# Kernel tuning notes

Hardware: AMD Instinct MI355X
Metric: run time of the kernel (lower is better)

The kernel has to match this reference:

```python
import jax, jax.numpy as jnp
import numpy as np

LN_EPS = 1e-5


def setup_inputs() -> dict:
    key = jax.random.key(0)
    k1, k2 = jax.random.split(key, 2)
    B, C, D, H, W = 2, 96, 32, 128, 128
    out_dim = 2 * C
    x = jax.random.normal(k1, (B, C, D, H, W), dtype=jnp.float32)
    # nn.Linear(8*C, out_dim, bias=False): weight shape (out_dim, 8*C)
    w = jax.random.normal(k2, (out_dim, 8 * C), dtype=jnp.float32) * 0.02
    gamma = jnp.ones((8 * C,), dtype=jnp.float32)
    beta = jnp.zeros((8 * C,), dtype=jnp.float32)
    return {"x": x, "w": w, "gamma": gamma, "beta": beta}


def reference(x, w, gamma, beta):
    B, C, D, H, W = x.shape
    D2, H2, W2 = D // 2, H // 2, W // 2
    # Strided 2x2x2 gather: reshape then move (dd,hh,ww) offsets next to C.
    # torch.cat order [x0..x7] = (dd,hh,ww) lexicographic, dd most significant,
    # with C channels per block -> layout (..., dd, hh, ww, C) flattened.
    xr = x.reshape(B, C, D2, 2, H2, 2, W2, 2)
    xr = xr.transpose(0, 2, 4, 6, 3, 5, 7, 1)  # (B, D2, H2, W2, dd, hh, ww, C)
    xf = xr.reshape(B, D2, H2, W2, 8 * C)
    # LayerNorm over last dim
    mu = jnp.mean(xf, axis=-1, keepdims=True)
    xc = xf - mu
    var = jnp.mean(xc * xc, axis=-1, keepdims=True)
    xn = xc * jax.lax.rsqrt(var + LN_EPS) * gamma + beta
    # Linear (no bias): y = xn @ w.T
    y = jnp.einsum('bdhwc,oc->bdhwo', xn, w)
    # back to channels-first (B, out_dim, D2, H2, W2)
    return y.transpose(0, 4, 1, 2, 3)
```

## Files before the change

### kernel.cpp

```cpp
#include <hip/hip_runtime.h>
#include <hip/hip_bf16.h>

typedef __attribute__((ext_vector_type(8))) short short8;
typedef __attribute__((ext_vector_type(4))) float f32x4;

#define LN_EPS 1e-5f

__device__ __forceinline__ unsigned short f2bf(float f) {
  union { float f; unsigned u; } v; v.f = f;
  unsigned r = v.u + 0x7FFFu + ((v.u >> 16) & 1u);
  return (unsigned short)(r >> 16);
}

__device__ __forceinline__ int a_addr(int row, int colb) {
  return row * 1536 + (colb ^ ((row & 7) << 4));
}


__global__ __launch_bounds__(256) void pm_prep(
    const float* __restrict__ w, const float* __restrict__ g,
    const float* __restrict__ be, unsigned short* __restrict__ wg,
    float* __restrict__ sb) {
  const int o = blockIdx.x;
  const int t = threadIdx.x;
  __shared__ float red[256][2];
  float sa = 0.f, ba = 0.f;
#pragma unroll
  for (int u = 0; u < 3; ++u) {
    int kp = t + 256 * u;
    int dh = kp / 192;
    int rem = kp - dh * 192;
    int c = rem >> 1, ww = rem & 1;
    int k = dh * 192 + ww * 96 + c;
    float wv = w[o * 768 + k];
    float v = wv * g[k];
    sa += v;
    ba += wv * be[k];
    int NT = o >> 4, ks = kp >> 5, qq = (kp >> 3) & 3, jj = kp & 7;
    wg[(((NT * 24 + ks) * 64) + qq * 16 + (o & 15)) * 8 + jj] = f2bf(v);
  }
  red[t][0] = sa; red[t][1] = ba;
  __syncthreads();
  if (t == 0) {
    float S = 0.f, B = 0.f;
    for (int i = 0; i < 256; ++i) { S += red[i][0]; B += red[i][1]; }
    sb[o] = S; sb[192 + o] = B;
  }
}

__global__ __launch_bounds__(256, 4) void pm_main(
    const float* __restrict__ x, const unsigned short* __restrict__ wg,
    const float* __restrict__ sb, float* __restrict__ out) {
  const int bid = blockIdx.x;
  const int wh = bid & 1;
  const int h2 = (bid >> 1) & 63;
  const int d2 = (bid >> 7) & 15;
  const int b = bid >> 11;
  const int t = threadIdx.x;
  const int lane = t & 63, wv = t >> 6;
  const int q = lane & 15, sc = lane >> 4;

  __shared__ __align__(16) unsigned char A_lds[32 * 1536];
  __shared__ float stats[32][2];
  __shared__ float part[4][32][2];

  const float* xb = x + (size_t)b * (96 * 32 * 128 * 128);
  const int dd = wv >> 1, hh = wv & 1;
  const int drow = 2 * d2 + dd, hrow = 2 * h2 + hh;

  float sum0 = 0.f, sq0 = 0.f, sum1 = 0.f, sq1 = 0.f;
#pragma unroll 4
  for (int cg = 0; cg < 12; ++cg) {
    int r0 = cg * 8 + 2 * sc;
    const float* p = xb + ((size_t)(r0 * 32 + drow) * 128 + hrow) * 128 + wh * 64 + 4 * q;
    float4 f0 = *(const float4*)p;
    float4 f1 = *(const float4*)(p + 32 * 128 * 128);
    sum0 += (f0.x + f0.y) + (f1.x + f1.y);
    sq0  += f0.x * f0.x + f0.y * f0.y + f1.x * f1.x + f1.y * f1.y;
    sum1 += (f0.z + f0.w) + (f1.z + f1.w);
    sq1  += f0.z * f0.z + f0.w * f0.w + f1.z * f1.z + f1.w * f1.w;
    int colb = 2 * (wv * 192 + cg * 16 + 4 * sc);
    ushort4 v0 = make_ushort4(f2bf(f0.x), f2bf(f0.y), f2bf(f1.x), f2bf(f1.y));
    ushort4 v1 = make_ushort4(f2bf(f0.z), f2bf(f0.w), f2bf(f1.z), f2bf(f1.w));
    *(ushort4*)&A_lds[a_addr(2 * q, colb)] = v0;
    *(ushort4*)&A_lds[a_addr(2 * q + 1, colb)] = v1;
  }
  sum0 += __shfl_xor(sum0, 16); sum0 += __shfl_xor(sum0, 32);
  sq0  += __shfl_xor(sq0, 16);  sq0  += __shfl_xor(sq0, 32);
  sum1 += __shfl_xor(sum1, 16); sum1 += __shfl_xor(sum1, 32);
  sq1  += __shfl_xor(sq1, 16);  sq1  += __shfl_xor(sq1, 32);
  if (sc == 0) {
    part[wv][2 * q][0] = sum0;     part[wv][2 * q][1] = sq0;
    part[wv][2 * q + 1][0] = sum1; part[wv][2 * q + 1][1] = sq1;
  }
  __syncthreads();
  if (t < 32) {
    float S = 0.f, Q = 0.f;
#pragma unroll
    for (int w4 = 0; w4 < 4; ++w4) { S += part[w4][t][0]; Q += part[w4][t][1]; }
    float mu = S * (1.f / 768.f);
    float var = Q * (1.f / 768.f) - mu * mu;
    float rs = rsqrtf(var + LN_EPS);
    stats[t][0] = rs;
    stats[t][1] = mu * rs;
  }
  __syncthreads();

  const int al = lane & 15, ah = lane >> 4;
  f32x4 acc[2][3];
#pragma unroll
  for (int mt = 0; mt < 2; ++mt)
#pragma unroll
    for (int nt = 0; nt < 3; ++nt) acc[mt][nt] = {0.f, 0.f, 0.f, 0.f};

  const short8* wgs = (const short8*)wg;
#pragma unroll 2
  for (int ks = 0; ks < 24; ++ks) {
    short8 afr[2];
#pragma unroll
    for (int mt = 0; mt < 2; ++mt)
      afr[mt] = *(const short8*)&A_lds[a_addr(mt * 16 + al, ks * 64 + ah * 16)];
#pragma unroll
    for (int nt = 0; nt < 3; ++nt) {
      short8 bfr = wgs[((wv * 3 + nt) * 24 + ks) * 64 + lane];
#pragma unroll
      for (int mt = 0; mt < 2; ++mt)
        acc[mt][nt] = __builtin_amdgcn_mfma_f32_16x16x32_bf16(afr[mt], bfr, acc[mt][nt], 0, 0, 0);
    }
  }

#pragma unroll
  for (int nt = 0; nt < 3; ++nt) {
    int o = wv * 48 + nt * 16 + al;
    float Sv = sb[o], Bv = sb[192 + o];
    float* ob = out + (((size_t)(b * 192 + o) * 16 + d2) * 64 + h2) * 64 + wh * 32;
#pragma unroll
    for (int mt = 0; mt < 2; ++mt) {
      int m0 = mt * 16 + ah * 4;
      float4 y;
      y.x = stats[m0 + 0][0] * acc[mt][nt][0] - stats[m0 + 0][1] * Sv + Bv;
      y.y = stats[m0 + 1][0] * acc[mt][nt][1] - stats[m0 + 1][1] * Sv + Bv;
      y.z = stats[m0 + 2][0] * acc[mt][nt][2] - stats[m0 + 2][1] * Sv + Bv;
      y.w = stats[m0 + 3][0] * acc[mt][nt][3] - stats[m0 + 3][1] * Sv + Bv;
      *(float4*)(ob + m0) = y;
    }
  }
}

extern "C" void kernel_launch(void* const* d_in, const int* in_sizes, int n_in,
                              void* d_out, int out_size, void* d_ws, size_t ws_size,
                              hipStream_t stream) {
  (void)in_sizes; (void)n_in; (void)out_size; (void)ws_size;
  const float* x  = (const float*)d_in[0];
  const float* w  = (const float*)d_in[1];
  const float* g  = (const float*)d_in[2];
  const float* be = (const float*)d_in[3];
  unsigned short* wg = (unsigned short*)d_ws;
  float* sb = (float*)((char*)d_ws + 192 * 768 * sizeof(unsigned short));
  pm_prep<<<192, 256, 0, stream>>>(w, g, be, wg, sb);
  pm_main<<<4096, 256, 0, stream>>>(x, wg, sb, (float*)d_out);
}
```

Measured before the change: 170.8 us.

## Pipeline x loads across four spatial phases and overlap them with MFMA

The main kernel now splits the 768-wide K dimension into four (dd,hh) phases. Each wave loads a channel slice for every phase and prefetches the next phase's global loads while it runs MFMAs on the current one. The B fragments for a phase are loaded up front, and the LayerNorm stats are computed in the last phase before the MFMAs. Occupancy is lowered to 3 blocks per SM to make room for the extra registers, and the prep kernel now uses a tree reduction. This hides global-load latency behind compute, at the cost of more syncs and register pressure.

```diff
diff --git a/kernel.cpp b/kernel.cpp
--- a/kernel.cpp
+++ b/kernel.cpp
@@ -41,14 +41,14 @@
   }
   red[t][0] = sa; red[t][1] = ba;
   __syncthreads();
-  if (t == 0) {
-    float S = 0.f, B = 0.f;
-    for (int i = 0; i < 256; ++i) { S += red[i][0]; B += red[i][1]; }
-    sb[o] = S; sb[192 + o] = B;
+  for (int s = 128; s > 0; s >>= 1) {
+    if (t < s) { red[t][0] += red[t + s][0]; red[t][1] += red[t + s][1]; }
+    __syncthreads();
   }
+  if (t == 0) { sb[o] = red[0][0]; sb[192 + o] = red[0][1]; }
 }
 
-__global__ __launch_bounds__(256, 4) void pm_main(
+__global__ __launch_bounds__(256, 3) void pm_main(
     const float* __restrict__ x, const unsigned short* __restrict__ wg,
     const float* __restrict__ sb, float* __restrict__ out) {
   const int bid = blockIdx.x;
@@ -61,73 +61,104 @@
   const int q = lane & 15, sc = lane >> 4;
 
   __shared__ __align__(16) unsigned char A_lds[32 * 1536];
+  __shared__ float part[4][32][2];
   __shared__ float stats[32][2];
-  __shared__ float part[4][32][2];
 
   const float* xb = x + (size_t)b * (96 * 32 * 128 * 128);
-  const int dd = wv >> 1, hh = wv & 1;
-  const int drow = 2 * d2 + dd, hrow = 2 * h2 + hh;
+  const int cp0 = wv * 12 + sc * 3;
+  const float* pc[3];
+#pragma unroll
+  for (int i = 0; i < 3; ++i)
+    pc[i] = xb + (size_t)(2 * (cp0 + i)) * 524288 + wh * 64 + 4 * q;
 
   float sum0 = 0.f, sq0 = 0.f, sum1 = 0.f, sq1 = 0.f;
-#pragma unroll 4
-  for (int cg = 0; cg < 12; ++cg) {
-    int r0 = cg * 8 + 2 * sc;
-    const float* p = xb + ((size_t)(r0 * 32 + drow) * 128 + hrow) * 128 + wh * 64 + 4 * q;
-    float4 f0 = *(const float4*)p;
-    float4 f1 = *(const float4*)(p + 32 * 128 * 128);
-    sum0 += (f0.x + f0.y) + (f1.x + f1.y);
-    sq0  += f0.x * f0.x + f0.y * f0.y + f1.x * f1.x + f1.y * f1.y;
-    sum1 += (f0.z + f0.w) + (f1.z + f1.w);
-    sq1  += f0.z * f0.z + f0.w * f0.w + f1.z * f1.z + f1.w * f1.w;
-    int colb = 2 * (wv * 192 + cg * 16 + 4 * sc);
-    ushort4 v0 = make_ushort4(f2bf(f0.x), f2bf(f0.y), f2bf(f1.x), f2bf(f1.y));
-    ushort4 v1 = make_ushort4(f2bf(f0.z), f2bf(f0.w), f2bf(f1.z), f2bf(f1.w));
-    *(ushort4*)&A_lds[a_addr(2 * q, colb)] = v0;
-    *(ushort4*)&A_lds[a_addr(2 * q + 1, colb)] = v1;
-  }
-  sum0 += __shfl_xor(sum0, 16); sum0 += __shfl_xor(sum0, 32);
-  sq0  += __shfl_xor(sq0, 16);  sq0  += __shfl_xor(sq0, 32);
-  sum1 += __shfl_xor(sum1, 16); sum1 += __shfl_xor(sum1, 32);
-  sq1  += __shfl_xor(sq1, 16);  sq1  += __shfl_xor(sq1, 32);
-  if (sc == 0) {
-    part[wv][2 * q][0] = sum0;     part[wv][2 * q][1] = sq0;
-    part[wv][2 * q + 1][0] = sum1; part[wv][2 * q + 1][1] = sq1;
-  }
-  __syncthreads();
-  if (t < 32) {
-    float S = 0.f, Q = 0.f;
+  float4 xa[3], xc[3];
+
+  auto issue = [&](int p) {
+    int off = (2 * d2 + (p >> 1)) * 16384 + (2 * h2 + (p & 1)) * 128;
 #pragma unroll
-    for (int w4 = 0; w4 < 4; ++w4) { S += part[w4][t][0]; Q += part[w4][t][1]; }
-    float mu = S * (1.f / 768.f);
-    float var = Q * (1.f / 768.f) - mu * mu;
-    float rs = rsqrtf(var + LN_EPS);
-    stats[t][0] = rs;
-    stats[t][1] = mu * rs;
-  }
-  __syncthreads();
+    for (int i = 0; i < 3; ++i) {
+      xa[i] = *(const float4*)(pc[i] + off);
+      xc[i] = *(const float4*)(pc[i] + 524288 + off);
+    }
+  };
+
+  auto consume = [&](int p) {
+#pragma unroll
+    for (int i = 0; i < 3; ++i) {
+      float4 f0 = xa[i], f1 = xc[i];
+      sum0 += (f0.x + f0.y) + (f1.x + f1.y);
+      sq0  += f0.x * f0.x + f0.y * f0.y + f1.x * f1.x + f1.y * f1.y;
+      sum1 += (f0.z + f0.w) + (f1.z + f1.w);
+      sq1  += f0.z * f0.z + f0.w * f0.w + f1.z * f1.z + f1.w * f1.w;
+      int colb = p * 384 + 8 * (cp0 + i);
+      *(ushort4*)&A_lds[a_addr(2 * q, colb)] =
+          make_ushort4(f2bf(f0.x), f2bf(f0.y), f2bf(f1.x), f2bf(f1.y));
+      *(ushort4*)&A_lds[a_addr(2 * q + 1, colb)] =
+          make_ushort4(f2bf(f0.z), f2bf(f0.w), f2bf(f1.z), f2bf(f1.w));
+    }
+  };
 
   const int al = lane & 15, ah = lane >> 4;
+  const short8* wgs = (const short8*)wg;
   f32x4 acc[2][3];
 #pragma unroll
   for (int mt = 0; mt < 2; ++mt)
 #pragma unroll
     for (int nt = 0; nt < 3; ++nt) acc[mt][nt] = {0.f, 0.f, 0.f, 0.f};
 
-  const short8* wgs = (const short8*)wg;
-#pragma unroll 2
-  for (int ks = 0; ks < 24; ++ks) {
-    short8 afr[2];
+  issue(0);
+
 #pragma unroll
-    for (int mt = 0; mt < 2; ++mt)
-      afr[mt] = *(const short8*)&A_lds[a_addr(mt * 16 + al, ks * 64 + ah * 16)];
+  for (int p = 0; p < 4; ++p) {
+    consume(p);
+    if (p == 3) {
+      sum0 += __shfl_xor(sum0, 16); sum0 += __shfl_xor(sum0, 32);
+      sq0  += __shfl_xor(sq0, 16);  sq0  += __shfl_xor(sq0, 32);
+      sum1 += __shfl_xor(sum1, 16); sum1 += __shfl_xor(sum1, 32);
+      sq1  += __shfl_xor(sq1, 16);  sq1  += __shfl_xor(sq1, 32);
+      if (sc == 0) {
+        part[wv][2 * q][0] = sum0;     part[wv][2 * q][1] = sq0;
+        part[wv][2 * q + 1][0] = sum1; part[wv][2 * q + 1][1] = sq1;
+      }
+    }
+    __syncthreads();
+
+    short8 bfr[6][3];
 #pragma unroll
-    for (int nt = 0; nt < 3; ++nt) {
-      short8 bfr = wgs[((wv * 3 + nt) * 24 + ks) * 64 + lane];
+    for (int ksi = 0; ksi < 6; ++ksi)
+#pragma unroll
+      for (int nt = 0; nt < 3; ++nt)
+        bfr[ksi][nt] = wgs[((wv * 3 + nt) * 24 + (p * 6 + ksi)) * 64 + lane];
+
+    if (p < 3) issue(p + 1);
+
+    if (p == 3) {
+      int row = t & 31;
+      float S = part[0][row][0] + part[1][row][0] + part[2][row][0] + part[3][row][0];
+      float Q = part[0][row][1] + part[1][row][1] + part[2][row][1] + part[3][row][1];
+      float mu = S * (1.f / 768.f);
+      float var = Q * (1.f / 768.f) - mu * mu;
+      float rs = rsqrtf(var + LN_EPS);
+      stats[row][0] = rs;
+      stats[row][1] = mu * rs;
+    }
+
+#pragma unroll
+    for (int ksi = 0; ksi < 6; ++ksi) {
+      int ks = p * 6 + ksi;
+      short8 afr[2];
 #pragma unroll
       for (int mt = 0; mt < 2; ++mt)
-        acc[mt][nt] = __builtin_amdgcn_mfma_f32_16x16x32_bf16(afr[mt], bfr, acc[mt][nt], 0, 0, 0);
+        afr[mt] = *(const short8*)&A_lds[a_addr(mt * 16 + al, ks * 64 + ah * 16)];
+#pragma unroll
+      for (int nt = 0; nt < 3; ++nt)
+#pragma unroll
+        for (int mt = 0; mt < 2; ++mt)
+          acc[mt][nt] = __builtin_amdgcn_mfma_f32_16x16x32_bf16(afr[mt], bfr[ksi][nt], acc[mt][nt], 0, 0, 0);
     }
   }
+  __syncthreads();
 
 #pragma unroll
   for (int nt = 0; nt < 3; ++nt) {
```

Result: faster. 149.9 us (-12.3%).
